# Kernel tuning notes

Hardware: AMD Instinct MI355X
Metric: run time of the kernel (lower is better)

## Reference

```python
import jax, jax.numpy as jnp
import numpy as np

VOCAB, D, A, NEG = 32000, 200, 20, 2
NUM_USERS, NUM_ITEMS = 100000, 50000
R, L, B, NNZ = 4096, 128, 1024, 20480
EPS = 1e-12

def _norm(x, axis):
    n = jnp.sqrt(jnp.sum(x * x, axis=axis, keepdims=True))
    return x / jnp.maximum(n, EPS)

def setup_inputs() -> dict:
    key = jax.random.key(0)
    ks = jax.random.split(key, 20)
    rows_u = jax.random.randint(ks[5], (NNZ,), 0, B)
    cols_u = jax.random.randint(ks[6], (NNZ,), 0, R)
    rows_i = jax.random.randint(ks[7], (NNZ,), 0, B)
    cols_i = jax.random.randint(ks[8], (NNZ,), 0, R)
    return {
        "historical_review": jax.random.randint(ks[0], (R, L), 0, VOCAB),
        "neg_review": jax.random.randint(ks[1], (R * NEG, L), 0, VOCAB),
        "user": jax.random.randint(ks[2], (B,), 0, NUM_USERS),
        "item": jax.random.randint(ks[3], (B,), 0, NUM_ITEMS),
        "label": jax.random.uniform(ks[4], (B,), jnp.float32, 1.0, 5.0),
        "user_histor_index": jnp.stack([rows_u, cols_u]),
        "user_histor_value": jax.random.uniform(ks[9], (NNZ,), jnp.float32),
        "item_histor_index": jnp.stack([rows_i, cols_i]),
        "item_histor_value": jax.random.uniform(ks[10], (NNZ,), jnp.float32),
        "word_emb": jax.random.normal(ks[11], (VOCAB, D), jnp.float32),
        "Wm": jax.random.normal(ks[12], (D, D), jnp.float32) * 0.05,
        "Ww": jax.random.normal(ks[13], (A, D), jnp.float32) * 0.05,
        "bw": jnp.zeros((A,), jnp.float32),
        "Wt": jax.random.normal(ks[14], (D, A), jnp.float32) * 0.05,
        "fc_w": jax.random.uniform(ks[15], (1, 2 * D), jnp.float32, -0.05, 0.05),
        "fc_b": jnp.zeros((1,), jnp.float32),
        "fm_V": jax.random.uniform(ks[16], (2 * D, 10), jnp.float32, -0.05, 0.05),
        "b_users": jax.random.uniform(ks[17], (NUM_USERS, 1), jnp.float32, 0.0, 0.1),
        "b_items": jax.random.uniform(ks[18], (NUM_ITEMS, 1), jnp.float32, 0.0, 0.1),
    }

def reference(historical_review, neg_review, user, item, label,
              user_histor_index, user_histor_value,
              item_histor_index, item_histor_value,
              word_emb, Wm, Ww, bw, Wt, fc_w, fc_b, fm_V, b_users, b_items):
    # ABAE attention over each review
    e_w = word_emb[historical_review]              # (R, L, D)
    y_s = jnp.mean(e_w, axis=1)                    # (R, D)
    z_n = jnp.mean(word_emb[neg_review], axis=1)   # (R*NEG, D)
    dx = jnp.einsum('rld,rd->rl', e_w @ Wm.T, y_s) # (R, L)
    ax = jax.nn.softmax(dx, axis=1)
    # Faithful to source: view(R, D, L) is a raw reshape, not a transpose.
    z_s = jnp.einsum('rdl,rl->rd', e_w.reshape(R, D, L), ax)  # (R, D)
    p_t = z_s @ Ww.T + bw                          # (R, A)
    r_s = p_t @ Wt.T                               # (R, D)
    # cosine margin ranking loss
    c1 = jnp.sum(_norm(r_s, 1) * _norm(z_s, 1), axis=-1)      # (R,)
    c1 = jnp.repeat(c1, NEG)                                   # (R*NEG,)
    c2 = jnp.sum(_norm(z_n.reshape(R, NEG, D), 2) * _norm(r_s, 1)[:, None, :], axis=-1).reshape(-1)
    abae_out_loss = jax.nn.relu(c2 - c1 + 1.0)     # margin=1, target=+1
    J_loss = jnp.mean(abae_out_loss)
    # aspect-matrix orthogonality regularizer
    Tn = _norm(Wt, 0)                              # normalize columns (dim=0)
    U_loss = jnp.mean((Tn.T @ Tn - jnp.eye(A, dtype=Wt.dtype)) ** 2)
    # sparse (B, R) @ (R, D) aggregation via segment_sum
    user_aspect_embed = jax.ops.segment_sum(
        user_histor_value[:, None] * r_s[user_histor_index[1]],
        user_histor_index[0], num_segments=B)      # (B, D)
    item_aspect_embed = jax.ops.segment_sum(
        item_histor_value[:, None] * r_s[item_histor_index[1]],
        item_histor_index[0], num_segments=B)      # (B, D)
    input_vec = jnp.concatenate([user_aspect_embed, item_aspect_embed], axis=1)  # (B, 2D)
    fm_linear = input_vec @ fc_w.T + fc_b          # (B, 1)
    fm_i1 = (input_vec @ fm_V) ** 2
    fm_i2 = (input_vec ** 2) @ (fm_V ** 2)
    # NOTE: faithful to source, the quadratic term is summed over the whole batch (scalar)
    fm_output = 0.5 * jnp.sum(fm_i1 - fm_i2) + fm_linear + b_users[user] + b_items[item]
    prediction = fm_output.squeeze(1)              # (B,)
    rating_loss = (prediction - label) ** 2
    mse_loss = jnp.mean(rating_loss)
    obj_loss = mse_loss + 0.01 * J_loss + 0.01 * U_loss
    return (obj_loss, rating_loss, abae_out_loss, prediction, user_aspect_embed, item_aspect_embed)
```

## Files before the change

### kernel.cpp

```cpp
#include <hip/hip_runtime.h>
#include <hip/hip_fp16.h>
#include <math.h>

#define R_TOT 4096
#define L_LEN 128
#define D_DIM 200
#define A_DIM 20
#define NEGK  2
#define B_SZ  1024
#define NNZ_C 20480
#define RN_TOT (R_TOT*NEGK)
#define S_TOT (R_TOT + RN_TOT)
#define VOCAB_C 32000
#define EPS_ 1e-12f
#define SLOT_CAP 64
#define NBUCK_BLK 160

__device__ __forceinline__ float4 unpack4(const uint2 u) {
  union { unsigned v; __half2 h; } c0, c1;
  c0.v = u.x; c1.v = u.y;
  const float2 f0 = __half22float2(c0.h);
  const float2 f1 = __half22float2(c1.h);
  return make_float4(f0.x, f0.y, f1.x, f1.y);
}

__global__ __launch_bounds__(256) void k_cast(
    const float* __restrict__ emb, ushort* __restrict__ emb_h, int* __restrict__ cnt)
{
  if (blockIdx.x == 0) {
    for (int i = threadIdx.x; i < 2*B_SZ; i += 256) cnt[i] = 0;
  }
  const int idx = blockIdx.x*256 + threadIdx.x;
  if (idx < (VOCAB_C*D_DIM)/4) {
    const float4 v = reinterpret_cast<const float4*>(emb)[idx];
    ushort4 o;
    o.x = __half_as_ushort(__float2half(v.x));
    o.y = __half_as_ushort(__float2half(v.y));
    o.z = __half_as_ushort(__float2half(v.z));
    o.w = __half_as_ushort(__float2half(v.w));
    reinterpret_cast<ushort4*>(emb_h)[idx] = o;
  }
}

__global__ __launch_bounds__(256, 8) void k_means2(
    const int* __restrict__ hist, const int* __restrict__ neg,
    const ushort* __restrict__ emb_h,
    float* __restrict__ ys_all, float* __restrict__ zn_all,
    const int* __restrict__ uidx, const float* __restrict__ uval,
    const int* __restrict__ iidx, const float* __restrict__ ival,
    int* __restrict__ cnt, int* __restrict__ scol, float* __restrict__ sval)
{
  const int sb = blockIdx.x;
  const int tid = threadIdx.x, lane = tid & 63, wv = tid >> 6;

  if (sb >= S_TOT) {
    const int g = (sb - S_TOT)*256 + tid;
    if (g < NNZ_C) {
      const int b = uidx[g];
      const int slot = atomicAdd(&cnt[b], 1);
      if (slot < SLOT_CAP) {
        scol[b*SLOT_CAP + slot] = uidx[NNZ_C + g];
        sval[b*SLOT_CAP + slot] = uval[g];
      }
    } else {
      const int g2 = g - NNZ_C;
      const int b = iidx[g2];
      const int slot = atomicAdd(&cnt[B_SZ + b], 1);
      if (slot < SLOT_CAP) {
        scol[(B_SZ + b)*SLOT_CAP + slot] = iidx[NNZ_C + g2];
        sval[(B_SZ + b)*SLOT_CAP + slot] = ival[g2];
      }
    }
    return;
  }

  __shared__ int widx[L_LEN];
  __shared__ __align__(16) float part[4][D_DIM];
  const bool is_pos = (sb < R_TOT);
  const int* src = is_pos ? (hist + (size_t)sb*L_LEN)
                          : (neg + (size_t)(sb - R_TOT)*L_LEN);
  if (tid < L_LEN) widx[tid] = src[tid];
  __syncthreads();

  const int lh = lane & 31;
  const int half = lane >> 5;
  float4 acc0 = {0.f,0.f,0.f,0.f}, acc1 = {0.f,0.f,0.f,0.f};
  for (int l = 2*wv; l < L_LEN; l += 8) {
    if (lh < 25) {
      const uint4 q = *reinterpret_cast<const uint4*>(
          emb_h + (size_t)widx[l + half]*D_DIM + 8*lh);
      const float4 v0 = unpack4(make_uint2(q.x, q.y));
      const float4 v1 = unpack4(make_uint2(q.z, q.w));
      acc0.x += v0.x; acc0.y += v0.y; acc0.z += v0.z; acc0.w += v0.w;
      acc1.x += v1.x; acc1.y += v1.y; acc1.z += v1.z; acc1.w += v1.w;
    }
  }
  acc0.x += __shfl_xor(acc0.x, 32); acc0.y += __shfl_xor(acc0.y, 32);
  acc0.z += __shfl_xor(acc0.z, 32); acc0.w += __shfl_xor(acc0.w, 32);
  acc1.x += __shfl_xor(acc1.x, 32); acc1.y += __shfl_xor(acc1.y, 32);
  acc1.z += __shfl_xor(acc1.z, 32); acc1.w += __shfl_xor(acc1.w, 32);
  if (lane < 25) {
    *reinterpret_cast<float4*>(&part[wv][8*lane])     = acc0;
    *reinterpret_cast<float4*>(&part[wv][8*lane + 4]) = acc1;
  }
  __syncthreads();
  float* dst = is_pos ? (ys_all + (size_t)sb*D_DIM)
                      : (zn_all + (size_t)(sb - R_TOT)*D_DIM);
  if (tid < D_DIM)
    dst[tid] = (part[0][tid] + part[1][tid] + part[2][tid] + part[3][tid]) * (1.0f/128.0f);
}

#define KB_RT 16
__global__ __launch_bounds__(256, 2) void k_matvec(
    const float* __restrict__ ys_all, const float* __restrict__ Wm,
    float* __restrict__ vv_all)
{
  __shared__ float ysl[KB_RT][D_DIM];
  const int r0 = blockIdx.x * KB_RT;
  const int tid = threadIdx.x;
  for (int i = tid; i < KB_RT*D_DIM; i += 256)
    ysl[i / D_DIM][i % D_DIM] = ys_all[(size_t)r0*D_DIM + i];
  __syncthreads();
  if (tid < D_DIM) {
    float acc[KB_RT];
    #pragma unroll
    for (int r = 0; r < KB_RT; ++r) acc[r] = 0.f;
    #pragma unroll 4
    for (int k = 0; k < D_DIM; ++k) {
      const float w = Wm[k*D_DIM + tid];
      #pragma unroll
      for (int r = 0; r < KB_RT; ++r) acc[r] += ysl[r][k] * w;
    }
    #pragma unroll
    for (int r = 0; r < KB_RT; ++r)
      vv_all[(size_t)(r0 + r)*D_DIM + tid] = acc[r];
  }
}

__global__ __launch_bounds__(256, 8) void k_attn(
    const int* __restrict__ hist, const ushort* __restrict__ emb_h,
    const float* __restrict__ vv_all, const float* __restrict__ Ww,
    const float* __restrict__ bw, const float* __restrict__ Wt,
    const float* __restrict__ zn_all,
    float* __restrict__ rs_out, float* __restrict__ abae)
{
  __shared__ int widx[L_LEN];
  __shared__ __align__(16) float ax[L_LEN];
  __shared__ __align__(16) float vvl[D_DIM];
  __shared__ float zs[D_DIM];
  __shared__ float ptile[160];
  __shared__ float red[44];
  const int r = blockIdx.x;
  const int tid = threadIdx.x, lane = tid & 63, wv = tid >> 6;

  if (tid < L_LEN) widx[tid] = hist[r*L_LEN + tid];
  if (tid < D_DIM) vvl[tid] = vv_all[(size_t)r*D_DIM + tid];
  __syncthreads();

  {
    const int lh = lane & 31;
    const int half = lane >> 5;
    float4 v8a = {0,0,0,0}, v8b = {0,0,0,0};
    if (lh < 25) {
      v8a = *reinterpret_cast<const float4*>(vvl + 8*lh);
      v8b = *reinterpret_cast<const float4*>(vvl + 8*lh + 4);
    }
    for (int l = 2*wv; l < L_LEN; l += 16) {
      float a0 = 0.f, a1 = 0.f;
      if (lh < 25) {
        const uint4 qA = *reinterpret_cast<const uint4*>(
            emb_h + (size_t)widx[l + half]*D_DIM + 8*lh);
        const uint4 qB = *reinterpret_cast<const uint4*>(
            emb_h + (size_t)widx[l + 8 + half]*D_DIM + 8*lh);
        const float4 eA0 = unpack4(make_uint2(qA.x, qA.y));
        const float4 eA1 = unpack4(make_uint2(qA.z, qA.w));
        const float4 eB0 = unpack4(make_uint2(qB.x, qB.y));
        const float4 eB1 = unpack4(make_uint2(qB.z, qB.w));
        a0 = eA0.x*v8a.x + eA0.y*v8a.y + eA0.z*v8a.z + eA0.w*v8a.w
           + eA1.x*v8b.x + eA1.y*v8b.y + eA1.z*v8b.z + eA1.w*v8b.w;
        a1 = eB0.x*v8a.x + eB0.y*v8a.y + eB0.z*v8a.z + eB0.w*v8a.w
           + eB1.x*v8b.x + eB1.y*v8b.y + eB1.z*v8b.z + eB1.w*v8b.w;
      }
      #pragma unroll
      for (int o = 16; o > 0; o >>= 1) {
        a0 += __shfl_xor(a0, o); a1 += __shfl_xor(a1, o);
      }
      if (lh == 0) { ax[l + half] = a0; ax[l + 8 + half] = a1; }
    }
  }
  __syncthreads();

  if (tid < 64) {
    float m = fmaxf(ax[tid], ax[tid+64]);
    #pragma unroll
    for (int o = 32; o > 0; o >>= 1) m = fmaxf(m, __shfl_xor(m, o));
    if (tid == 0) red[0] = m;
  }
  __syncthreads();
  const float M = red[0];
  if (tid < L_LEN) ax[tid] = expf(ax[tid] - M);
  __syncthreads();
  if (tid < 64) {
    float s = ax[tid] + ax[tid+64];
    #pragma unroll
    for (int o = 32; o > 0; o >>= 1) s += __shfl_xor(s, o);
    if (tid == 0) red[1] = s;
  }
  __syncthreads();
  const float Sinv = 1.0f / red[1];
  if (tid < L_LEN) ax[tid] *= Sinv;
  __syncthreads();

  {
    const int lq = lane & 15;
    const int quad = lane >> 4;
    const float4 ax8a = *reinterpret_cast<const float4*>(ax + 8*lq);
    const float4 ax8b = *reinterpret_cast<const float4*>(ax + 8*lq + 4);
    int dq = wv;
    for (; dq < 48; dq += 8) {
      const int d0 = 4*dq + quad;
      const int d1 = 4*(dq + 4) + quad;
      const int f0 = (d0 << 7) + 8*lq;
      const int f1 = (d1 << 7) + 8*lq;
      const uint4 qA = *reinterpret_cast<const uint4*>(
          emb_h + (size_t)widx[f0/200]*D_DIM + (f0 % 200));
      const uint4 qB = *reinterpret_cast<const uint4*>(
          emb_h + (size_t)widx[f1/200]*D_DIM + (f1 % 200));
      const float4 eA0 = unpack4(make_uint2(qA.x, qA.y));
      const float4 eA1 = unpack4(make_uint2(qA.z, qA.w));
      const float4 eB0 = unpack4(make_uint2(qB.x, qB.y));
      const float4 eB1 = unpack4(make_uint2(qB.z, qB.w));
      float a0 = eA0.x*ax8a.x + eA0.y*ax8a.y + eA0.z*ax8a.z + eA0.w*ax8a.w
               + eA1.x*ax8b.x + eA1.y*ax8b.y + eA1.z*ax8b.z + eA1.w*ax8b.w;
      float a1 = eB0.x*ax8a.x + eB0.y*ax8a.y + eB0.z*ax8a.z + eB0.w*ax8a.w
               + eB1.x*ax8b.x + eB1.y*ax8b.y + eB1.z*ax8b.z + eB1.w*ax8b.w;
      #pragma unroll
      for (int o = 8; o > 0; o >>= 1) {
        a0 += __shfl_xor(a0, o); a1 += __shfl_xor(a1, o);
      }
      if (lq == 0) { zs[d0] = a0; zs[d1] = a1; }
    }
    if (dq < 50) {
      const int d = 4*dq + quad;
      const int f = (d << 7) + 8*lq;
      const uint4 q = *reinterpret_cast<const uint4*>(
          emb_h + (size_t)widx[f/200]*D_DIM + (f % 200));
      const float4 e0 = unpack4(make_uint2(q.x, q.y));
      const float4 e1 = unpack4(make_uint2(q.z, q.w));
      float a = e0.x*ax8a.x + e0.y*ax8a.y + e0.z*ax8a.z + e0.w*ax8a.w
              + e1.x*ax8b.x + e1.y*ax8b.y + e1.z*ax8b.z + e1.w*ax8b.w;
      #pragma unroll
      for (int o = 8; o > 0; o >>= 1) a += __shfl_xor(a, o);
      if (lq == 0) zs[d] = a;
    }
  }
  __syncthreads();

  if (tid < 160) {
    const int a = tid % 20, j = tid / 20;
    float s = 0.f;
    #pragma unroll
    for (int i = 0; i < 25; ++i) {
      const int d = j + 8*i;
      s += zs[d] * Ww[a*D_DIM + d];
    }
    ptile[tid] = s;
  }
  __syncthreads();
  if (tid < A_DIM) {
    float s = bw[tid];
    #pragma unroll
    for (int j = 0; j < 8; ++j) s += ptile[j*20 + tid];
    red[2 + tid] = s;
  }
  __syncthreads();

  float rsd = 0.f, zsd = 0.f, zn0 = 0.f, zn1 = 0.f;
  if (tid < D_DIM) {
    float acc = 0.f;
    #pragma unroll
    for (int a = 0; a < A_DIM; ++a) acc += red[2+a] * Wt[tid*A_DIM + a];
    rsd = acc; zsd = zs[tid];
    rs_out[(size_t)r*D_DIM + tid] = acc;
    zn0 = zn_all[(size_t)(2*r)*D_DIM + tid];
    zn1 = zn_all[(size_t)(2*r + 1)*D_DIM + tid];
  }
  float a0 = rsd*rsd, a1 = zsd*zsd, a2 = rsd*zsd;
  float b0 = zn0*zn0, b1 = zn0*rsd, b2 = zn1*zn1, b3 = zn1*rsd;
  #pragma unroll
  for (int o = 32; o > 0; o >>= 1) {
    a0 += __shfl_xor(a0, o); a1 += __shfl_xor(a1, o); a2 += __shfl_xor(a2, o);
    b0 += __shfl_xor(b0, o); b1 += __shfl_xor(b1, o);
    b2 += __shfl_xor(b2, o); b3 += __shfl_xor(b3, o);
  }
  if ((tid & 63) == 0) {
    red[12+wv] = a0; red[16+wv] = a1; red[20+wv] = a2;
    red[24+wv] = b0; red[28+wv] = b1; red[32+wv] = b2; red[36+wv] = b3;
  }
  __syncthreads();
  if (tid == 0) {
    const float s0 = red[12]+red[13]+red[14]+red[15];
    const float s1 = red[16]+red[17]+red[18]+red[19];
    const float s2 = red[20]+red[21]+red[22]+red[23];
    const float t0 = red[24]+red[25]+red[26]+red[27];
    const float t1 = red[28]+red[29]+red[30]+red[31];
    const float t2 = red[32]+red[33]+red[34]+red[35];
    const float t3 = red[36]+red[37]+red[38]+red[39];
    const float nr = fmaxf(sqrtf(s0), EPS_);
    const float nz = fmaxf(sqrtf(s1), EPS_);
    const float c1 = s2 / (nr * nz);
    const float c2a = t1 / (fmaxf(sqrtf(t0), EPS_) * nr);
    const float c2b = t3 / (fmaxf(sqrtf(t2), EPS_) * nr);
    abae[2*r]     = fmaxf(c2a - c1 + 1.0f, 0.0f);
    abae[2*r + 1] = fmaxf(c2b - c1 + 1.0f, 0.0f);
  }
}

__global__ __launch_bounds__(512) void k_aggfm(
    const int* __restrict__ cnt, const int* __restrict__ scol,
    const float* __restrict__ sval, const float* __restrict__ rs,
    const float* __restrict__ fcw, const float* __restrict__ V,
    float* __restrict__ uae, float* __restrict__ iae,
    float* __restrict__ linb, float* __restrict__ quadb)
{
  __shared__ __align__(16) float ivec[2*D_DIM];
  __shared__ float redw[8];
  __shared__ float qpart[10];
  const int b = blockIdx.x;
  const int tid = threadIdx.x, lane = tid & 63, wv = tid >> 6;

  if (tid < D_DIM) {
    int n = cnt[b]; n = n < SLOT_CAP ? n : SLOT_CAP;
    const int* cols = scol + (size_t)b*SLOT_CAP;
    const float* vals = sval + (size_t)b*SLOT_CAP;
    float acc = 0.f;
    for (int j = 0; j < n; ++j) acc += vals[j] * rs[(size_t)cols[j]*D_DIM + tid];
    ivec[tid] = acc;
    uae[(size_t)b*D_DIM + tid] = acc;
  } else if (tid >= 256 && tid < 256 + D_DIM) {
    const int t = tid - 256;
    int n = cnt[B_SZ + b]; n = n < SLOT_CAP ? n : SLOT_CAP;
    const int* cols = scol + (size_t)(B_SZ + b)*SLOT_CAP;
    const float* vals = sval + (size_t)(B_SZ + b)*SLOT_CAP;
    float acc = 0.f;
    for (int j = 0; j < n; ++j) acc += vals[j] * rs[(size_t)cols[j]*D_DIM + t];
    ivec[D_DIM + t] = acc;
    iae[(size_t)b*D_DIM + t] = acc;
  }
  __syncthreads();

  float lv = 0.f;
  if (tid < 2*D_DIM) lv = ivec[tid] * fcw[tid];
  #pragma unroll
  for (int o = 32; o > 0; o >>= 1) lv += __shfl_xor(lv, o);
  if (lane == 0) redw[wv] = lv;

  {
    const int k = wv;
    float s1 = 0.f, s2 = 0.f;
    for (int f = lane; f < 2*D_DIM; f += 64) {
      const float x = ivec[f];
      const float vk = V[f*10 + k];
      s1 += x*vk; s2 += x*x*vk*vk;
    }
    #pragma unroll
    for (int o = 32; o > 0; o >>= 1) { s1 += __shfl_xor(s1,o); s2 += __shfl_xor(s2,o); }
    if (lane == 0) qpart[k] = s1*s1 - s2;
  }
  if (wv < 2) {
    const int k = 8 + wv;
    float s1 = 0.f, s2 = 0.f;
    for (int f = lane; f < 2*D_DIM; f += 64) {
      const float x = ivec[f];
      const float vk = V[f*10 + k];
      s1 += x*vk; s2 += x*x*vk*vk;
    }
    #pragma unroll
    for (int o = 32; o > 0; o >>= 1) { s1 += __shfl_xor(s1,o); s2 += __shfl_xor(s2,o); }
    if (lane == 0) qpart[k] = s1*s1 - s2;
  }
  __syncthreads();
  if (tid == 0) {
    float lin = 0.f;
    #pragma unroll
    for (int i = 0; i < 8; ++i) lin += redw[i];
    float q = 0.f;
    #pragma unroll
    for (int i = 0; i < 10; ++i) q += qpart[i];
    linb[b] = lin; quadb[b] = q;
  }
}

__global__ __launch_bounds__(1024) void k_final2(
    const float* __restrict__ quadb, const float* __restrict__ linb,
    const float* __restrict__ fcb, const int* __restrict__ user,
    const int* __restrict__ item, const float* __restrict__ busers,
    const float* __restrict__ bitems, const float* __restrict__ label,
    const float* __restrict__ Wt, const float* __restrict__ abae,
    float* __restrict__ pred, float* __restrict__ rl, float* __restrict__ obj)
{
  __shared__ float sA[16], sB[16], sC[16];
  __shared__ float cninv[A_DIM];
  __shared__ float quad_s;
  const int tid = threadIdx.x;
  const int lane = tid & 63;
  const int wv = tid >> 6;

  float q = quadb[tid];
  #pragma unroll
  for (int o = 32; o > 0; o >>= 1) q += __shfl_xor(q, o);
  if (lane == 0) sA[wv] = q;

  if (tid < A_DIM) {
    float s = 0.f;
    for (int d = 0; d < D_DIM; ++d) { const float w = Wt[d*A_DIM + tid]; s += w*w; }
    cninv[tid] = 1.0f / fmaxf(sqrtf(s), EPS_);
  }
  __syncthreads();
  if (wv == 0) {
    float s = (lane < 16) ? sA[lane] : 0.f;
    #pragma unroll
    for (int o = 32; o > 0; o >>= 1) s += __shfl_xor(s, o);
    if (lane == 0) quad_s = s;
  }
  __syncthreads();

  const float p = 0.5f*quad_s + linb[tid] + fcb[0]
                + busers[user[tid]] + bitems[item[tid]];
  pred[tid] = p;
  const float dd = p - label[tid];
  const float myrl = dd*dd;
  rl[tid] = myrl;

  float u = 0.f;
  if (tid < 400) {
    const int a = tid / 20, c = tid % 20;
    float dot = 0.f;
    for (int d = 0; d < D_DIM; ++d) dot += Wt[d*A_DIM + a]*Wt[d*A_DIM + c];
    const float g = dot*cninv[a]*cninv[c] - (a==c ? 1.0f : 0.0f);
    u = g*g;
  }
  float js = 0.f;
  #pragma unroll
  for (int j = 0; j < 8; ++j) js += abae[tid + 1024*j];
  float ms = myrl;

  #pragma unroll
  for (int o = 32; o > 0; o >>= 1) {
    u += __shfl_xor(u,o); js += __shfl_xor(js,o); ms += __shfl_xor(ms,o);
  }
  if (lane == 0) { sA[wv] = u; sB[wv] = js; sC[wv] = ms; }
  __syncthreads();
  if (tid == 0) {
    float U = 0.f, J = 0.f, Ms = 0.f;
    for (int i = 0; i < 16; ++i) { U += sA[i]; J += sB[i]; Ms += sC[i]; }
    obj[0] = Ms/1024.0f + 0.01f*(J/8192.0f) + 0.01f*(U/400.0f);
  }
}

extern "C" void kernel_launch(void* const* d_in, const int* in_sizes, int n_in,
                              void* d_out, int out_size, void* d_ws, size_t ws_size,
                              hipStream_t stream) {
  const int*   hist   = (const int*)  d_in[0];
  const int*   neg    = (const int*)  d_in[1];
  const int*   user   = (const int*)  d_in[2];
  const int*   item   = (const int*)  d_in[3];
  const float* label  = (const float*)d_in[4];
  const int*   uidx   = (const int*)  d_in[5];
  const float* uval   = (const float*)d_in[6];
  const int*   iidx   = (const int*)  d_in[7];
  const float* ival   = (const float*)d_in[8];
  const float* emb    = (const float*)d_in[9];
  const float* Wm     = (const float*)d_in[10];
  const float* Ww     = (const float*)d_in[11];
  const float* bw     = (const float*)d_in[12];
  const float* Wt     = (const float*)d_in[13];
  const float* fcw    = (const float*)d_in[14];
  const float* fcb    = (const float*)d_in[15];
  const float* V      = (const float*)d_in[16];
  const float* busers = (const float*)d_in[17];
  const float* bitems = (const float*)d_in[18];

  float* out  = (float*)d_out;
  float* obj  = out;
  float* rl   = out + 1;
  float* abae = out + 1 + B_SZ;
  float* pred = out + 1 + B_SZ + RN_TOT;
  float* uae  = pred + B_SZ;
  float* iae  = uae + (size_t)B_SZ*D_DIM;

  float* ws     = (float*)d_ws;
  float* rs     = ws;
  float* ys_all = rs + (size_t)R_TOT*D_DIM;
  float* zn_all = ys_all + (size_t)R_TOT*D_DIM;
  float* vv_all = zn_all + (size_t)RN_TOT*D_DIM;
  float* linb   = vv_all + (size_t)R_TOT*D_DIM;
  float* quadb  = linb + B_SZ;
  float* sval   = quadb + B_SZ;
  int*   scol   = (int*)(sval + (size_t)2*B_SZ*SLOT_CAP);
  int*   cnt    = scol + (size_t)2*B_SZ*SLOT_CAP;
  ushort* emb_h = (ushort*)(cnt + 2*B_SZ);

  const int cast_blocks = (VOCAB_C*D_DIM/4 + 255)/256;

  k_cast  <<<cast_blocks, 256, 0, stream>>>(emb, emb_h, cnt);
  k_means2<<<S_TOT + NBUCK_BLK, 256, 0, stream>>>(hist, neg, emb_h,
                                                  ys_all, zn_all,
                                                  uidx, uval, iidx, ival,
                                                  cnt, scol, sval);
  k_matvec<<<R_TOT/KB_RT, 256, 0, stream>>>(ys_all, Wm, vv_all);
  k_attn  <<<R_TOT, 256, 0, stream>>>(hist, emb_h, vv_all, Ww, bw, Wt,
                                      zn_all, rs, abae);
  k_aggfm <<<B_SZ, 512, 0, stream>>>(cnt, scol, sval, rs, fcw, V,
                                     uae, iae, linb, quadb);
  k_final2<<<1, 1024, 0, stream>>>(quadb, linb, fcb, user, item, busers, bitems,
                                   label, Wt, abae, pred, rl, obj);
}
```

Before: 313.7 us.

## Fuse positive-review mean, Wm matvec and attention into one LDS-cached kernel

Positive-review mean pooling, the Wm projection and the attention kernel are merged into a single 512-thread block per review. Each block gathers its 128 fp16 embedding rows into shared memory once and reuses them for the mean, the attention logits and the weighted sum, instead of gathering them three times from global memory. This also removes the ys_all and vv_all round trips and one launch. The costs are about 51KB of LDS per block, which limits occupancy, and a per-block 200x200 matvec that rereads Wm with no amortisation across rows.

```diff
diff --git a/kernel.cpp b/kernel.cpp
--- a/kernel.cpp
+++ b/kernel.cpp
@@ -10,7 +10,6 @@
 #define B_SZ  1024
 #define NNZ_C 20480
 #define RN_TOT (R_TOT*NEGK)
-#define S_TOT (R_TOT + RN_TOT)
 #define VOCAB_C 32000
 #define EPS_ 1e-12f
 #define SLOT_CAP 64
@@ -42,10 +41,9 @@
   }
 }
 
-__global__ __launch_bounds__(256, 8) void k_means2(
-    const int* __restrict__ hist, const int* __restrict__ neg,
-    const ushort* __restrict__ emb_h,
-    float* __restrict__ ys_all, float* __restrict__ zn_all,
+__global__ __launch_bounds__(256, 8) void k_means_neg(
+    const int* __restrict__ neg, const ushort* __restrict__ emb_h,
+    float* __restrict__ zn_all,
     const int* __restrict__ uidx, const float* __restrict__ uval,
     const int* __restrict__ iidx, const float* __restrict__ ival,
     int* __restrict__ cnt, int* __restrict__ scol, float* __restrict__ sval)
@@ -53,8 +51,8 @@
   const int sb = blockIdx.x;
   const int tid = threadIdx.x, lane = tid & 63, wv = tid >> 6;
 
-  if (sb >= S_TOT) {
-    const int g = (sb - S_TOT)*256 + tid;
+  if (sb >= RN_TOT) {
+    const int g = (sb - RN_TOT)*256 + tid;
     if (g < NNZ_C) {
       const int b = uidx[g];
       const int slot = atomicAdd(&cnt[b], 1);
@@ -76,9 +74,7 @@
 
   __shared__ int widx[L_LEN];
   __shared__ __align__(16) float part[4][D_DIM];
-  const bool is_pos = (sb < R_TOT);
-  const int* src = is_pos ? (hist + (size_t)sb*L_LEN)
-                          : (neg + (size_t)(sb - R_TOT)*L_LEN);
+  const int* src = neg + (size_t)sb*L_LEN;
   if (tid < L_LEN) widx[tid] = src[tid];
   __syncthreads();
 
@@ -104,57 +100,72 @@
     *reinterpret_cast<float4*>(&part[wv][8*lane + 4]) = acc1;
   }
   __syncthreads();
-  float* dst = is_pos ? (ys_all + (size_t)sb*D_DIM)
-                      : (zn_all + (size_t)(sb - R_TOT)*D_DIM);
+  float* dst = zn_all + (size_t)sb*D_DIM;
   if (tid < D_DIM)
     dst[tid] = (part[0][tid] + part[1][tid] + part[2][tid] + part[3][tid]) * (1.0f/128.0f);
 }
 
-#define KB_RT 16
-__global__ __launch_bounds__(256, 2) void k_matvec(
-    const float* __restrict__ ys_all, const float* __restrict__ Wm,
-    float* __restrict__ vv_all)
-{
-  __shared__ float ysl[KB_RT][D_DIM];
-  const int r0 = blockIdx.x * KB_RT;
-  const int tid = threadIdx.x;
-  for (int i = tid; i < KB_RT*D_DIM; i += 256)
-    ysl[i / D_DIM][i % D_DIM] = ys_all[(size_t)r0*D_DIM + i];
-  __syncthreads();
-  if (tid < D_DIM) {
-    float acc[KB_RT];
-    #pragma unroll
-    for (int r = 0; r < KB_RT; ++r) acc[r] = 0.f;
-    #pragma unroll 4
-    for (int k = 0; k < D_DIM; ++k) {
-      const float w = Wm[k*D_DIM + tid];
-      #pragma unroll
-      for (int r = 0; r < KB_RT; ++r) acc[r] += ysl[r][k] * w;
-    }
-    #pragma unroll
-    for (int r = 0; r < KB_RT; ++r)
-      vv_all[(size_t)(r0 + r)*D_DIM + tid] = acc[r];
-  }
-}
-
-__global__ __launch_bounds__(256, 8) void k_attn(
+__global__ __launch_bounds__(512, 4) void k_fused(
     const int* __restrict__ hist, const ushort* __restrict__ emb_h,
-    const float* __restrict__ vv_all, const float* __restrict__ Ww,
+    const float* __restrict__ Wm, const float* __restrict__ Ww,
     const float* __restrict__ bw, const float* __restrict__ Wt,
     const float* __restrict__ zn_all,
     float* __restrict__ rs_out, float* __restrict__ abae)
 {
+  __shared__ __align__(16) ushort ew[L_LEN*D_DIM];
+  __shared__ __align__(16) float stg[16][D_DIM];
+  __shared__ __align__(16) float ax[L_LEN];
+  __shared__ __align__(16) float vv[D_DIM];
+  __shared__ __align__(16) float zs[D_DIM];
+  __shared__ float ptile[160];
+  __shared__ float red[80];
   __shared__ int widx[L_LEN];
-  __shared__ __align__(16) float ax[L_LEN];
-  __shared__ __align__(16) float vvl[D_DIM];
-  __shared__ float zs[D_DIM];
-  __shared__ float ptile[160];
-  __shared__ float red[44];
+
   const int r = blockIdx.x;
   const int tid = threadIdx.x, lane = tid & 63, wv = tid >> 6;
 
   if (tid < L_LEN) widx[tid] = hist[r*L_LEN + tid];
-  if (tid < D_DIM) vvl[tid] = vv_all[(size_t)r*D_DIM + tid];
+  __syncthreads();
+
+  {
+    const int c5 = tid & 31;
+    const int j  = tid >> 5;
+    if (c5 < 25) {
+      float p0=0.f,p1=0.f,p2=0.f,p3=0.f,p4=0.f,p5=0.f,p6=0.f,p7=0.f;
+      #pragma unroll
+      for (int k = 0; k < 8; ++k) {
+        const int l = j + 16*k;
+        const uint4 q = *reinterpret_cast<const uint4*>(
+            emb_h + (size_t)widx[l]*D_DIM + 8*c5);
+        *reinterpret_cast<uint4*>(ew + l*D_DIM + 8*c5) = q;
+        const float4 v0 = unpack4(make_uint2(q.x, q.y));
+        const float4 v1 = unpack4(make_uint2(q.z, q.w));
+        p0 += v0.x; p1 += v0.y; p2 += v0.z; p3 += v0.w;
+        p4 += v1.x; p5 += v1.y; p6 += v1.z; p7 += v1.w;
+      }
+      *reinterpret_cast<float4*>(&stg[j][8*c5])     = make_float4(p0,p1,p2,p3);
+      *reinterpret_cast<float4*>(&stg[j][8*c5 + 4]) = make_float4(p4,p5,p6,p7);
+    }
+  }
+  __syncthreads();
+
+  if (tid < D_DIM) {
+    float s = 0.f;
+    #pragma unroll
+    for (int j2 = 0; j2 < 16; ++j2) s += stg[j2][tid];
+    zs[tid] = s * (1.0f/128.0f);
+  }
+  __syncthreads();
+
+  if (tid < 400) {
+    const int k = tid % 200, h = tid / 200;
+    float acc = 0.f;
+    #pragma unroll 4
+    for (int d = 100*h; d < 100*h + 100; ++d) acc += zs[d] * Wm[d*D_DIM + k];
+    stg[h][k] = acc;
+  }
+  __syncthreads();
+  if (tid < D_DIM) vv[tid] = stg[0][tid] + stg[1][tid];
   __syncthreads();
 
   {
@@ -162,30 +173,21 @@
     const int half = lane >> 5;
     float4 v8a = {0,0,0,0}, v8b = {0,0,0,0};
     if (lh < 25) {
-      v8a = *reinterpret_cast<const float4*>(vvl + 8*lh);
-      v8b = *reinterpret_cast<const float4*>(vvl + 8*lh + 4);
+      v8a = *reinterpret_cast<const float4*>(vv + 8*lh);
+      v8b = *reinterpret_cast<const float4*>(vv + 8*lh + 4);
     }
     for (int l = 2*wv; l < L_LEN; l += 16) {
-      float a0 = 0.f, a1 = 0.f;
+      float a0 = 0.f;
       if (lh < 25) {
-        const uint4 qA = *reinterpret_cast<const uint4*>(
-            emb_h + (size_t)widx[l + half]*D_DIM + 8*lh);
-        const uint4 qB = *reinterpret_cast<const uint4*>(
-            emb_h + (size_t)widx[l + 8 + half]*D_DIM + 8*lh);
-        const float4 eA0 = unpack4(make_uint2(qA.x, qA.y));
-        const float4 eA1 = unpack4(make_uint2(qA.z, qA.w));
-        const float4 eB0 = unpack4(make_uint2(qB.x, qB.y));
-        const float4 eB1 = unpack4(make_uint2(qB.z, qB.w));
-        a0 = eA0.x*v8a.x + eA0.y*v8a.y + eA0.z*v8a.z + eA0.w*v8a.w
-           + eA1.x*v8b.x + eA1.y*v8b.y + eA1.z*v8b.z + eA1.w*v8b.w;
-        a1 = eB0.x*v8a.x + eB0.y*v8a.y + eB0.z*v8a.z + eB0.w*v8a.w
-           + eB1.x*v8b.x + eB1.y*v8b.y + eB1.z*v8b.z + eB1.w*v8b.w;
+        const uint4 q = *reinterpret_cast<const uint4*>(ew + (l + half)*D_DIM + 8*lh);
+        const float4 e0 = unpack4(make_uint2(q.x, q.y));
+        const float4 e1 = unpack4(make_uint2(q.z, q.w));
+        a0 = e0.x*v8a.x + e0.y*v8a.y + e0.z*v8a.z + e0.w*v8a.w
+           + e1.x*v8b.x + e1.y*v8b.y + e1.z*v8b.z + e1.w*v8b.w;
       }
       #pragma unroll
-      for (int o = 16; o > 0; o >>= 1) {
-        a0 += __shfl_xor(a0, o); a1 += __shfl_xor(a1, o);
-      }
-      if (lh == 0) { ax[l + half] = a0; ax[l + 8 + half] = a1; }
+      for (int o = 16; o > 0; o >>= 1) a0 += __shfl_xor(a0, o);
+      if (lh == 0) ax[l + half] = a0;
     }
   }
   __syncthreads();
@@ -216,42 +218,17 @@
     const int quad = lane >> 4;
     const float4 ax8a = *reinterpret_cast<const float4*>(ax + 8*lq);
     const float4 ax8b = *reinterpret_cast<const float4*>(ax + 8*lq + 4);
-    int dq = wv;
-    for (; dq < 48; dq += 8) {
+    for (int dq = wv; dq < 50; dq += 8) {
       const int d0 = 4*dq + quad;
-      const int d1 = 4*(dq + 4) + quad;
       const int f0 = (d0 << 7) + 8*lq;
-      const int f1 = (d1 << 7) + 8*lq;
-      const uint4 qA = *reinterpret_cast<const uint4*>(
-          emb_h + (size_t)widx[f0/200]*D_DIM + (f0 % 200));
-      const uint4 qB = *reinterpret_cast<const uint4*>(
-          emb_h + (size_t)widx[f1/200]*D_DIM + (f1 % 200));
-      const float4 eA0 = unpack4(make_uint2(qA.x, qA.y));
-      const float4 eA1 = unpack4(make_uint2(qA.z, qA.w));
-      const float4 eB0 = unpack4(make_uint2(qB.x, qB.y));
-      const float4 eB1 = unpack4(make_uint2(qB.z, qB.w));
-      float a0 = eA0.x*ax8a.x + eA0.y*ax8a.y + eA0.z*ax8a.z + eA0.w*ax8a.w
-               + eA1.x*ax8b.x + eA1.y*ax8b.y + eA1.z*ax8b.z + eA1.w*ax8b.w;
-      float a1 = eB0.x*ax8a.x + eB0.y*ax8a.y + eB0.z*ax8a.z + eB0.w*ax8a.w
-               + eB1.x*ax8b.x + eB1.y*ax8b.y + eB1.z*ax8b.z + eB1.w*ax8b.w;
-      #pragma unroll
-      for (int o = 8; o > 0; o >>= 1) {
-        a0 += __shfl_xor(a0, o); a1 += __shfl_xor(a1, o);
-      }
-      if (lq == 0) { zs[d0] = a0; zs[d1] = a1; }
-    }
-    if (dq < 50) {
-      const int d = 4*dq + quad;
-      const int f = (d << 7) + 8*lq;
-      const uint4 q = *reinterpret_cast<const uint4*>(
-          emb_h + (size_t)widx[f/200]*D_DIM + (f % 200));
+      const uint4 q = *reinterpret_cast<const uint4*>(ew + f0);
       const float4 e0 = unpack4(make_uint2(q.x, q.y));
       const float4 e1 = unpack4(make_uint2(q.z, q.w));
       float a = e0.x*ax8a.x + e0.y*ax8a.y + e0.z*ax8a.z + e0.w*ax8a.w
               + e1.x*ax8b.x + e1.y*ax8b.y + e1.z*ax8b.z + e1.w*ax8b.w;
       #pragma unroll
       for (int o = 8; o > 0; o >>= 1) a += __shfl_xor(a, o);
-      if (lq == 0) zs[d] = a;
+      if (lq == 0) zs[d0] = a;
     }
   }
   __syncthreads();
@@ -294,18 +271,17 @@
     b2 += __shfl_xor(b2, o); b3 += __shfl_xor(b3, o);
   }
   if ((tid & 63) == 0) {
-    red[12+wv] = a0; red[16+wv] = a1; red[20+wv] = a2;
-    red[24+wv] = b0; red[28+wv] = b1; red[32+wv] = b2; red[36+wv] = b3;
+    red[22+wv] = a0; red[30+wv] = a1; red[38+wv] = a2;
+    red[46+wv] = b0; red[54+wv] = b1; red[62+wv] = b2; red[70+wv] = b3;
   }
   __syncthreads();
   if (tid == 0) {
-    const float s0 = red[12]+red[13]+red[14]+red[15];
-    const float s1 = red[16]+red[17]+red[18]+red[19];
-    const float s2 = red[20]+red[21]+red[22]+red[23];
-    const float t0 = red[24]+red[25]+red[26]+red[27];
-    const float t1 = red[28]+red[29]+red[30]+red[31];
-    const float t2 = red[32]+red[33]+red[34]+red[35];
-    const float t3 = red[36]+red[37]+red[38]+red[39];
+    float s0=0.f,s1=0.f,s2=0.f,t0=0.f,t1=0.f,t2=0.f,t3=0.f;
+    #pragma unroll
+    for (int i = 0; i < 8; ++i) {
+      s0 += red[22+i]; s1 += red[30+i]; s2 += red[38+i];
+      t0 += red[46+i]; t1 += red[54+i]; t2 += red[62+i]; t3 += red[70+i];
+    }
     const float nr = fmaxf(sqrtf(s0), EPS_);
     const float nz = fmaxf(sqrtf(s1), EPS_);
     const float c1 = s2 / (nr * nz);
@@ -491,10 +467,8 @@
 
   float* ws     = (float*)d_ws;
   float* rs     = ws;
-  float* ys_all = rs + (size_t)R_TOT*D_DIM;
-  float* zn_all = ys_all + (size_t)R_TOT*D_DIM;
-  float* vv_all = zn_all + (size_t)RN_TOT*D_DIM;
-  float* linb   = vv_all + (size_t)R_TOT*D_DIM;
+  float* zn_all = rs + (size_t)R_TOT*D_DIM;
+  float* linb   = zn_all + (size_t)RN_TOT*D_DIM;
   float* quadb  = linb + B_SZ;
   float* sval   = quadb + B_SZ;
   int*   scol   = (int*)(sval + (size_t)2*B_SZ*SLOT_CAP);
@@ -503,16 +477,14 @@
 
   const int cast_blocks = (VOCAB_C*D_DIM/4 + 255)/256;
 
-  k_cast  <<<cast_blocks, 256, 0, stream>>>(emb, emb_h, cnt);
-  k_means2<<<S_TOT + NBUCK_BLK, 256, 0, stream>>>(hist, neg, emb_h,
-                                                  ys_all, zn_all,
-                                                  uidx, uval, iidx, ival,
-                                                  cnt, scol, sval);
-  k_matvec<<<R_TOT/KB_RT, 256, 0, stream>>>(ys_all, Wm, vv_all);
-  k_attn  <<<R_TOT, 256, 0, stream>>>(hist, emb_h, vv_all, Ww, bw, Wt,
-                                      zn_all, rs, abae);
-  k_aggfm <<<B_SZ, 512, 0, stream>>>(cnt, scol, sval, rs, fcw, V,
-                                     uae, iae, linb, quadb);
-  k_final2<<<1, 1024, 0, stream>>>(quadb, linb, fcb, user, item, busers, bitems,
-                                   label, Wt, abae, pred, rl, obj);
-}
+  k_cast     <<<cast_blocks, 256, 0, stream>>>(emb, emb_h, cnt);
+  k_means_neg<<<RN_TOT + NBUCK_BLK, 256, 0, stream>>>(neg, emb_h, zn_all,
+                                                      uidx, uval, iidx, ival,
+                                                      cnt, scol, sval);
+  k_fused    <<<R_TOT, 512, 0, stream>>>(hist, emb_h, Wm, Ww, bw, Wt,
+                                         zn_all, rs, abae);
+  k_aggfm    <<<B_SZ, 512, 0, stream>>>(cnt, scol, sval, rs, fcw, V,
+                                        uae, iae, linb, quadb);
+  k_final2   <<<1, 1024, 0, stream>>>(quadb, linb, fcb, user, item, busers, bitems,
+                                      label, Wt, abae, pred, rl, obj);
+}
```

Result: slower. 357.7 us (+14.0%).

## Stage gathered embeddings in LDS for attention and unroll mean gathers

Applied to the files above, without the earlier changes.

k_attn now runs with 512 threads. The half-precision embedding rows it gathers for the score pass are stored in a 51KB shared buffer, so the weighted-sum pass reads them from LDS instead of gathering them from global memory a second time. k_means2 now issues four independent row loads per iteration across 8 row-groups, adding memory-level parallelism, and reduces eight partial sums. The large LDS footprint limits how many k_attn blocks fit per CU, and the reduction slot layout in red was changed to handle 8 waves.

```diff
diff --git a/kernel.cpp b/kernel.cpp
--- a/kernel.cpp
+++ b/kernel.cpp
@@ -51,7 +51,7 @@
     int* __restrict__ cnt, int* __restrict__ scol, float* __restrict__ sval)
 {
   const int sb = blockIdx.x;
-  const int tid = threadIdx.x, lane = tid & 63, wv = tid >> 6;
+  const int tid = threadIdx.x;
 
   if (sb >= S_TOT) {
     const int g = (sb - S_TOT)*256 + tid;
@@ -75,39 +75,50 @@
   }
 
   __shared__ int widx[L_LEN];
-  __shared__ __align__(16) float part[4][D_DIM];
+  __shared__ __align__(16) float part[8][D_DIM];
   const bool is_pos = (sb < R_TOT);
   const int* src = is_pos ? (hist + (size_t)sb*L_LEN)
                           : (neg + (size_t)(sb - R_TOT)*L_LEN);
   if (tid < L_LEN) widx[tid] = src[tid];
   __syncthreads();
 
-  const int lh = lane & 31;
-  const int half = lane >> 5;
-  float4 acc0 = {0.f,0.f,0.f,0.f}, acc1 = {0.f,0.f,0.f,0.f};
-  for (int l = 2*wv; l < L_LEN; l += 8) {
-    if (lh < 25) {
-      const uint4 q = *reinterpret_cast<const uint4*>(
-          emb_h + (size_t)widx[l + half]*D_DIM + 8*lh);
-      const float4 v0 = unpack4(make_uint2(q.x, q.y));
-      const float4 v1 = unpack4(make_uint2(q.z, q.w));
-      acc0.x += v0.x; acc0.y += v0.y; acc0.z += v0.z; acc0.w += v0.w;
-      acc1.x += v1.x; acc1.y += v1.y; acc1.z += v1.z; acc1.w += v1.w;
-    }
-  }
-  acc0.x += __shfl_xor(acc0.x, 32); acc0.y += __shfl_xor(acc0.y, 32);
-  acc0.z += __shfl_xor(acc0.z, 32); acc0.w += __shfl_xor(acc0.w, 32);
-  acc1.x += __shfl_xor(acc1.x, 32); acc1.y += __shfl_xor(acc1.y, 32);
-  acc1.z += __shfl_xor(acc1.z, 32); acc1.w += __shfl_xor(acc1.w, 32);
-  if (lane < 25) {
-    *reinterpret_cast<float4*>(&part[wv][8*lane])     = acc0;
-    *reinterpret_cast<float4*>(&part[wv][8*lane + 4]) = acc1;
+  const int c5 = tid & 31;
+  const int j  = tid >> 5;
+  float4 sA = {0.f,0.f,0.f,0.f}, sB = {0.f,0.f,0.f,0.f};
+  if (c5 < 25) {
+    const size_t coff = 8*c5;
+    #pragma unroll
+    for (int k0 = 0; k0 < 16; k0 += 4) {
+      const uint4 q0 = *reinterpret_cast<const uint4*>(
+          emb_h + (size_t)widx[j + 8*(k0+0)]*D_DIM + coff);
+      const uint4 q1 = *reinterpret_cast<const uint4*>(
+          emb_h + (size_t)widx[j + 8*(k0+1)]*D_DIM + coff);
+      const uint4 q2 = *reinterpret_cast<const uint4*>(
+          emb_h + (size_t)widx[j + 8*(k0+2)]*D_DIM + coff);
+      const uint4 q3 = *reinterpret_cast<const uint4*>(
+          emb_h + (size_t)widx[j + 8*(k0+3)]*D_DIM + coff);
+      float4 e;
+      e = unpack4(make_uint2(q0.x,q0.y)); sA.x+=e.x; sA.y+=e.y; sA.z+=e.z; sA.w+=e.w;
+      e = unpack4(make_uint2(q0.z,q0.w)); sB.x+=e.x; sB.y+=e.y; sB.z+=e.z; sB.w+=e.w;
+      e = unpack4(make_uint2(q1.x,q1.y)); sA.x+=e.x; sA.y+=e.y; sA.z+=e.z; sA.w+=e.w;
+      e = unpack4(make_uint2(q1.z,q1.w)); sB.x+=e.x; sB.y+=e.y; sB.z+=e.z; sB.w+=e.w;
+      e = unpack4(make_uint2(q2.x,q2.y)); sA.x+=e.x; sA.y+=e.y; sA.z+=e.z; sA.w+=e.w;
+      e = unpack4(make_uint2(q2.z,q2.w)); sB.x+=e.x; sB.y+=e.y; sB.z+=e.z; sB.w+=e.w;
+      e = unpack4(make_uint2(q3.x,q3.y)); sA.x+=e.x; sA.y+=e.y; sA.z+=e.z; sA.w+=e.w;
+      e = unpack4(make_uint2(q3.z,q3.w)); sB.x+=e.x; sB.y+=e.y; sB.z+=e.z; sB.w+=e.w;
+    }
+    *reinterpret_cast<float4*>(&part[j][8*c5])     = sA;
+    *reinterpret_cast<float4*>(&part[j][8*c5 + 4]) = sB;
   }
   __syncthreads();
   float* dst = is_pos ? (ys_all + (size_t)sb*D_DIM)
                       : (zn_all + (size_t)(sb - R_TOT)*D_DIM);
-  if (tid < D_DIM)
-    dst[tid] = (part[0][tid] + part[1][tid] + part[2][tid] + part[3][tid]) * (1.0f/128.0f);
+  if (tid < D_DIM) {
+    float a = 0.f;
+    #pragma unroll
+    for (int j2 = 0; j2 < 8; ++j2) a += part[j2][tid];
+    dst[tid] = a * (1.0f/128.0f);
+  }
 }
 
 #define KB_RT 16
@@ -137,55 +148,62 @@
   }
 }
 
-__global__ __launch_bounds__(256, 8) void k_attn(
+__global__ __launch_bounds__(512, 6) void k_attn(
     const int* __restrict__ hist, const ushort* __restrict__ emb_h,
-    const float* __restrict__ vv_all, const float* __restrict__ Ww,
-    const float* __restrict__ bw, const float* __restrict__ Wt,
-    const float* __restrict__ zn_all,
+    const float* __restrict__ vv_all,
+    const float* __restrict__ Ww, const float* __restrict__ bw,
+    const float* __restrict__ Wt, const float* __restrict__ zn_all,
     float* __restrict__ rs_out, float* __restrict__ abae)
 {
-  __shared__ int widx[L_LEN];
+  __shared__ __align__(16) ushort ew[L_LEN*D_DIM];
   __shared__ __align__(16) float ax[L_LEN];
-  __shared__ __align__(16) float vvl[D_DIM];
-  __shared__ float zs[D_DIM];
-  __shared__ float ptile[160];
-  __shared__ float red[44];
+  __shared__ __align__(16) float zs[D_DIM];
+  __shared__ __align__(16) float ubuf[240];
+  int*   widx  = reinterpret_cast<int*>(ubuf);
+  float* ptile = ubuf;
+  float* red   = ubuf + 160;
+
   const int r = blockIdx.x;
   const int tid = threadIdx.x, lane = tid & 63, wv = tid >> 6;
 
   if (tid < L_LEN) widx[tid] = hist[r*L_LEN + tid];
-  if (tid < D_DIM) vvl[tid] = vv_all[(size_t)r*D_DIM + tid];
   __syncthreads();
 
   {
-    const int lh = lane & 31;
-    const int half = lane >> 5;
+    const int c5 = tid & 31;
+    const int j  = tid >> 5;
     float4 v8a = {0,0,0,0}, v8b = {0,0,0,0};
-    if (lh < 25) {
-      v8a = *reinterpret_cast<const float4*>(vvl + 8*lh);
-      v8b = *reinterpret_cast<const float4*>(vvl + 8*lh + 4);
-    }
-    for (int l = 2*wv; l < L_LEN; l += 16) {
-      float a0 = 0.f, a1 = 0.f;
-      if (lh < 25) {
-        const uint4 qA = *reinterpret_cast<const uint4*>(
-            emb_h + (size_t)widx[l + half]*D_DIM + 8*lh);
-        const uint4 qB = *reinterpret_cast<const uint4*>(
-            emb_h + (size_t)widx[l + 8 + half]*D_DIM + 8*lh);
-        const float4 eA0 = unpack4(make_uint2(qA.x, qA.y));
-        const float4 eA1 = unpack4(make_uint2(qA.z, qA.w));
-        const float4 eB0 = unpack4(make_uint2(qB.x, qB.y));
-        const float4 eB1 = unpack4(make_uint2(qB.z, qB.w));
-        a0 = eA0.x*v8a.x + eA0.y*v8a.y + eA0.z*v8a.z + eA0.w*v8a.w
-           + eA1.x*v8b.x + eA1.y*v8b.y + eA1.z*v8b.z + eA1.w*v8b.w;
-        a1 = eB0.x*v8a.x + eB0.y*v8a.y + eB0.z*v8a.z + eB0.w*v8a.w
-           + eB1.x*v8b.x + eB1.y*v8b.y + eB1.z*v8b.z + eB1.w*v8b.w;
+    if (c5 < 25) {
+      v8a = *reinterpret_cast<const float4*>(vv_all + (size_t)r*D_DIM + 8*c5);
+      v8b = *reinterpret_cast<const float4*>(vv_all + (size_t)r*D_DIM + 8*c5 + 4);
+    }
+    float p0=0.f,p1=0.f,p2=0.f,p3=0.f,p4=0.f,p5=0.f,p6=0.f,p7=0.f;
+    if (c5 < 25) {
+      const size_t coff = 8*c5;
+      #pragma unroll
+      for (int k = 0; k < 8; ++k) {
+        const int l = j + 16*k;
+        const uint4 q = *reinterpret_cast<const uint4*>(
+            emb_h + (size_t)widx[l]*D_DIM + coff);
+        *reinterpret_cast<uint4*>(ew + l*D_DIM + coff) = q;
+        const float4 e0 = unpack4(make_uint2(q.x, q.y));
+        const float4 e1 = unpack4(make_uint2(q.z, q.w));
+        const float d = e0.x*v8a.x + e0.y*v8a.y + e0.z*v8a.z + e0.w*v8a.w
+                      + e1.x*v8b.x + e1.y*v8b.y + e1.z*v8b.z + e1.w*v8b.w;
+        if (k==0) p0=d; else if (k==1) p1=d; else if (k==2) p2=d; else if (k==3) p3=d;
+        else if (k==4) p4=d; else if (k==5) p5=d; else if (k==6) p6=d; else p7=d;
       }
-      #pragma unroll
-      for (int o = 16; o > 0; o >>= 1) {
-        a0 += __shfl_xor(a0, o); a1 += __shfl_xor(a1, o);
-      }
-      if (lh == 0) { ax[l + half] = a0; ax[l + 8 + half] = a1; }
+    }
+    #pragma unroll
+    for (int o = 16; o > 0; o >>= 1) {
+      p0 += __shfl_xor(p0, o); p1 += __shfl_xor(p1, o);
+      p2 += __shfl_xor(p2, o); p3 += __shfl_xor(p3, o);
+      p4 += __shfl_xor(p4, o); p5 += __shfl_xor(p5, o);
+      p6 += __shfl_xor(p6, o); p7 += __shfl_xor(p7, o);
+    }
+    if (c5 == 0) {
+      ax[j]      = p0; ax[j + 16]  = p1; ax[j + 32]  = p2; ax[j + 48]  = p3;
+      ax[j + 64] = p4; ax[j + 80]  = p5; ax[j + 96]  = p6; ax[j + 112] = p7;
     }
   }
   __syncthreads();
@@ -216,42 +234,17 @@
     const int quad = lane >> 4;
     const float4 ax8a = *reinterpret_cast<const float4*>(ax + 8*lq);
     const float4 ax8b = *reinterpret_cast<const float4*>(ax + 8*lq + 4);
-    int dq = wv;
-    for (; dq < 48; dq += 8) {
+    for (int dq = wv; dq < 50; dq += 8) {
       const int d0 = 4*dq + quad;
-      const int d1 = 4*(dq + 4) + quad;
       const int f0 = (d0 << 7) + 8*lq;
-      const int f1 = (d1 << 7) + 8*lq;
-      const uint4 qA = *reinterpret_cast<const uint4*>(
-          emb_h + (size_t)widx[f0/200]*D_DIM + (f0 % 200));
-      const uint4 qB = *reinterpret_cast<const uint4*>(
-          emb_h + (size_t)widx[f1/200]*D_DIM + (f1 % 200));
-      const float4 eA0 = unpack4(make_uint2(qA.x, qA.y));
-      const float4 eA1 = unpack4(make_uint2(qA.z, qA.w));
-      const float4 eB0 = unpack4(make_uint2(qB.x, qB.y));
-      const float4 eB1 = unpack4(make_uint2(qB.z, qB.w));
-      float a0 = eA0.x*ax8a.x + eA0.y*ax8a.y + eA0.z*ax8a.z + eA0.w*ax8a.w
-               + eA1.x*ax8b.x + eA1.y*ax8b.y + eA1.z*ax8b.z + eA1.w*ax8b.w;
-      float a1 = eB0.x*ax8a.x + eB0.y*ax8a.y + eB0.z*ax8a.z + eB0.w*ax8a.w
-               + eB1.x*ax8b.x + eB1.y*ax8b.y + eB1.z*ax8b.z + eB1.w*ax8b.w;
-      #pragma unroll
-      for (int o = 8; o > 0; o >>= 1) {
-        a0 += __shfl_xor(a0, o); a1 += __shfl_xor(a1, o);
-      }
-      if (lq == 0) { zs[d0] = a0; zs[d1] = a1; }
-    }
-    if (dq < 50) {
-      const int d = 4*dq + quad;
-      const int f = (d << 7) + 8*lq;
-      const uint4 q = *reinterpret_cast<const uint4*>(
-          emb_h + (size_t)widx[f/200]*D_DIM + (f % 200));
+      const uint4 q = *reinterpret_cast<const uint4*>(ew + f0);
       const float4 e0 = unpack4(make_uint2(q.x, q.y));
       const float4 e1 = unpack4(make_uint2(q.z, q.w));
       float a = e0.x*ax8a.x + e0.y*ax8a.y + e0.z*ax8a.z + e0.w*ax8a.w
               + e1.x*ax8b.x + e1.y*ax8b.y + e1.z*ax8b.z + e1.w*ax8b.w;
       #pragma unroll
       for (int o = 8; o > 0; o >>= 1) a += __shfl_xor(a, o);
-      if (lq == 0) zs[d] = a;
+      if (lq == 0) zs[d0] = a;
     }
   }
   __syncthreads();
@@ -294,18 +287,17 @@
     b2 += __shfl_xor(b2, o); b3 += __shfl_xor(b3, o);
   }
   if ((tid & 63) == 0) {
-    red[12+wv] = a0; red[16+wv] = a1; red[20+wv] = a2;
-    red[24+wv] = b0; red[28+wv] = b1; red[32+wv] = b2; red[36+wv] = b3;
+    red[22+wv] = a0; red[30+wv] = a1; red[38+wv] = a2;
+    red[46+wv] = b0; red[54+wv] = b1; red[62+wv] = b2; red[70+wv] = b3;
   }
   __syncthreads();
   if (tid == 0) {
-    const float s0 = red[12]+red[13]+red[14]+red[15];
-    const float s1 = red[16]+red[17]+red[18]+red[19];
-    const float s2 = red[20]+red[21]+red[22]+red[23];
-    const float t0 = red[24]+red[25]+red[26]+red[27];
-    const float t1 = red[28]+red[29]+red[30]+red[31];
-    const float t2 = red[32]+red[33]+red[34]+red[35];
-    const float t3 = red[36]+red[37]+red[38]+red[39];
+    float s0=0.f,s1=0.f,s2=0.f,t0=0.f,t1=0.f,t2=0.f,t3=0.f;
+    #pragma unroll
+    for (int i = 0; i < 8; ++i) {
+      s0 += red[22+i]; s1 += red[30+i]; s2 += red[38+i];
+      t0 += red[46+i]; t1 += red[54+i]; t2 += red[62+i]; t3 += red[70+i];
+    }
     const float nr = fmaxf(sqrtf(s0), EPS_);
     const float nz = fmaxf(sqrtf(s1), EPS_);
     const float c1 = s2 / (nr * nz);
@@ -509,7 +501,7 @@
                                                   uidx, uval, iidx, ival,
                                                   cnt, scol, sval);
   k_matvec<<<R_TOT/KB_RT, 256, 0, stream>>>(ys_all, Wm, vv_all);
-  k_attn  <<<R_TOT, 256, 0, stream>>>(hist, emb_h, vv_all, Ww, bw, Wt,
+  k_attn  <<<R_TOT, 512, 0, stream>>>(hist, emb_h, vv_all, Ww, bw, Wt,
                                       zn_all, rs, abae);
   k_aggfm <<<B_SZ, 512, 0, stream>>>(cnt, scol, sval, rs, fcw, V,
                                      uae, iae, linb, quadb);
```

Measured after the change: 312.5 us. No clear change (-0.4%).
